# Kernel optimization log

Measured on AMD Instinct MI355X. Metric: run time of the kernel, lower is better.

The kernel has to match this reference:

```python
import jax, jax.numpy as jnp
import numpy as np

N, E = 20000, 160000
D_NODE_IN, D_EDGE_IN = 256, 64
D = 128          # node/edge feature dim
H = 256          # edge hidden dim
T = 17           # number of keypoint types
EDGE_STEPS, NODE_STEPS = 2, 1


def _w(k, shape):
    return jax.random.normal(k, shape, dtype=jnp.float32) / np.sqrt(shape[-2] if len(shape) > 1 else shape[-1]).astype(np.float32)


def setup_inputs() -> dict:
    key = jax.random.key(0)
    ks = iter(jax.random.split(key, 40))
    inp = {
        'x': jax.random.normal(next(ks), (N, D_NODE_IN), dtype=jnp.float32),
        'edge_attr': jax.random.normal(next(ks), (E, D_EDGE_IN), dtype=jnp.float32),
        'edge_index': jax.random.randint(next(ks), (2, E), 0, N),
        'node_types': jax.random.randint(next(ks), (N,), 0, T),
        # type-routed node embedding: 17 stacked 2-layer MLPs 256->128->128
        'ne_w1': _w(next(ks), (T, D_NODE_IN, D)), 'ne_b1': jnp.zeros((T, D)),
        'ne_w2': _w(next(ks), (T, D, D)),         'ne_b2': jnp.zeros((T, D)),
        # edge embedding 64->128->128
        'ee_w1': _w(next(ks), (D_EDGE_IN, D)), 'ee_b1': jnp.zeros((D,)),
        'ee_w2': _w(next(ks), (D, D)),         'ee_b2': jnp.zeros((D,)),
        # MPLayer edge MLP: [x_i, x_j, e] with skip -> (2*2D + 2D)=768 -> 256 -> 128
        'me_w1': _w(next(ks), (4 * D + 2 * D, H)), 'me_b1': jnp.zeros((H,)),
        'me_w2': _w(next(ks), (H, D)),             'me_b2': jnp.zeros((D,)),
        # MPLayer node update: [x(skip 2D), agg(D)] -> 128
        'mn_w1': _w(next(ks), (2 * D + D, D)), 'mn_b1': jnp.zeros((D,)),
        # classifiers
        'ec_w1': _w(next(ks), (D, D)), 'ec_b1': jnp.zeros((D,)),
        'ec_w2': _w(next(ks), (D, 1)), 'ec_b2': jnp.zeros((1,)),
        'nc_w1': _w(next(ks), (D, D)), 'nc_b1': jnp.zeros((D,)),
        'nc_w2': _w(next(ks), (D, 1)), 'nc_b2': jnp.zeros((1,)),
        'cc_w1': _w(next(ks), (D, D)), 'cc_b1': jnp.zeros((D,)),
        'cc_w2': _w(next(ks), (D, T)), 'cc_b2': jnp.zeros((T,)),
    }
    return inp


def _mlp2(x, w1, b1, w2, b2):
    return jax.nn.relu(x @ w1 + b1) @ w2 + b2


def reference(x, edge_attr, edge_index, node_types,
              ne_w1, ne_b1, ne_w2, ne_b2,
              ee_w1, ee_b1, ee_w2, ee_b2,
              me_w1, me_b1, me_w2, me_b2,
              mn_w1, mn_b1,
              ec_w1, ec_b1, ec_w2, ec_b2,
              nc_w1, nc_b1, nc_w2, nc_b2,
              cc_w1, cc_b1, cc_w2, cc_b2):
    n = x.shape[0]
    # NodeMlpType: run all 17 MLPs, select by node type (same math as masked dispatch)
    h = jax.nn.relu(jnp.einsum('nd,tdk->tnk', x, ne_w1) + ne_b1[:, None, :])   # [T,N,D]
    o = jnp.einsum('tnk,tkm->tnm', h, ne_w2) + ne_b2[:, None, :]               # [T,N,D]
    nf0 = o[node_types, jnp.arange(n)]                                          # [N,D]
    ef0 = _mlp2(edge_attr, ee_w1, ee_b1, ee_w2, ee_b2)                          # [E,D]

    src, dst = edge_index[0], edge_index[1]

    def mp_step(nf, ef):
        nf_c = jnp.concatenate([nf0, nf], axis=1)                               # skip concat [N,2D]
        ef_c = jnp.concatenate([ef0, ef], axis=1)                               # [E,2D]
        m = jnp.concatenate([nf_c[dst], nf_c[src], ef_c], axis=1)               # [E,6D]
        e_new = _mlp2(m, me_w1, me_b1, me_w2, me_b2)                            # [E,D]
        agg = jax.ops.segment_sum(e_new, dst, num_segments=n)                   # aggr='add'
        nf_new = jnp.concatenate([nf_c, agg], axis=1) @ mn_w1 + mn_b1           # [N,D]
        return nf_new, e_new

    nf, ef = nf0, ef0
    for _ in range(EDGE_STEPS):
        nf, ef = mp_step(nf, ef)
    pred_edge = _mlp2(ef, ec_w1, ec_b1, ec_w2, ec_b2).squeeze(-1)               # [E]
    for _ in range(NODE_STEPS):
        nf, ef = mp_step(nf, ef)
    pred_node = _mlp2(nf, nc_w1, nc_b1, nc_w2, nc_b2).squeeze(-1)               # [N]
    pred_class = _mlp2(nf, cc_w1, cc_b1, cc_w2, cc_b2)                          # [N,T]
    return (pred_edge, pred_node, pred_class, nf, ef)
```

## Files before the change

### kernel.cpp

```cpp
#include <hip/hip_runtime.h>
#include <hip/hip_bf16.h>

#define N_NODES 20000
#define N_EDGES 160000
#define DIN_NODE 256
#define DIN_EDGE 64
#define DF 128
#define HH 256
#define TT 17
#define NE_PAD_SLOTS 20544

typedef __attribute__((ext_vector_type(8))) short short8v;
typedef __attribute__((ext_vector_type(4))) float f32x4;

__device__ __forceinline__ unsigned short f2bf(float f) {
  unsigned int u = __builtin_bit_cast(unsigned int, f);
  u += 0x7FFFu + ((u >> 16) & 1u);
  return (unsigned short)(u >> 16);
}

__device__ __forceinline__ float bf2f(unsigned short u) {
  return __builtin_bit_cast(float, (unsigned int)u << 16);
}

__device__ __forceinline__ short8v pack8(float4 a, float4 b) {
  short8v o;
  o[0] = (short)f2bf(a.x); o[1] = (short)f2bf(a.y);
  o[2] = (short)f2bf(a.z); o[3] = (short)f2bf(a.w);
  o[4] = (short)f2bf(b.x); o[5] = (short)f2bf(b.y);
  o[6] = (short)f2bf(b.z); o[7] = (short)f2bf(b.w);
  return o;
}

__global__ __launch_bounds__(256) void k_pack_w(
    const float* __restrict__ w, unsigned short* __restrict__ out,
    int Kdim, int Ndim, int batch) {
  const int tile = blockIdx.x * 4 + (threadIdx.x >> 6);
  const int l = threadIdx.x & 63;
  const int ntTiles = Ndim >> 4;
  const int tilesPer = (Kdim >> 5) * ntTiles;
  if (tile >= tilesPer * batch) return;
  const int bt = tile / tilesPer;
  const int rr = tile - bt * tilesPer;
  const int kt = rr / ntTiles, nt = rr % ntTiles;
  const float* wb = w + (size_t)bt * Kdim * Ndim;
  const int col = (nt << 4) + (l & 15);
  const int k0 = (kt << 5) + ((l >> 4) << 3);
  unsigned short* o = out + (((size_t)tile << 6) + l) * 8;
#pragma unroll
  for (int j = 0; j < 8; ++j) o[j] = f2bf(wb[(size_t)(k0 + j) * Ndim + col]);
}

__global__ void k_count(const int* __restrict__ types, int* __restrict__ cnt) {
  const int n = blockIdx.x * 256 + threadIdx.x;
  if (n < N_NODES) atomicAdd(&cnt[types[n]], 1);
}
__global__ void k_prefix(const int* __restrict__ cnt, int* __restrict__ poff,
                         int* __restrict__ woff) {
  if (threadIdx.x == 0) {
    int cur = 0;
    for (int t = 0; t < TT; ++t) {
      poff[t] = cur; woff[t] = cur;
      cur += (cnt[t] + 31) & ~31;
    }
  }
}
__global__ void k_scatter(const int* __restrict__ types, int* __restrict__ woff,
                          int* __restrict__ bucket) {
  const int n = blockIdx.x * 256 + threadIdx.x;
  if (n < N_NODES) {
    const int pos = atomicAdd(&woff[types[n]], 1);
    bucket[pos] = n;
  }
}

__global__ __launch_bounds__(256) void k_node_embed_mfma(
    const float* __restrict__ x, const int* __restrict__ bucket,
    const int* __restrict__ types,
    const unsigned short* __restrict__ wp1, const float* __restrict__ b1,
    const unsigned short* __restrict__ wp2, const float* __restrict__ b2,
    unsigned short* __restrict__ nf0b) {
  __shared__ __align__(16) unsigned char A[32 * 512];
  __shared__ __align__(16) unsigned char Hb[32 * 256];
  __shared__ int sn[32];
  const int t = threadIdx.x;
  const int r0 = blockIdx.x * 32;
  if (t < 32) sn[t] = bucket[r0 + t];
  __syncthreads();
  if (sn[0] < 0) return;
  const int ty = types[sn[0]];

#pragma unroll
  for (int j = 0; j < 4; ++j) {
    const int q = j * 256 + t;
    const int i = q >> 5, c = q & 31;
    const int nd = sn[i];
    short8v o;
    if (nd >= 0) {
      const float* xr = x + (size_t)nd * DIN_NODE + c * 8;
      o = pack8(*reinterpret_cast<const float4*>(xr),
                *reinterpret_cast<const float4*>(xr + 4));
    } else {
#pragma unroll
      for (int k = 0; k < 8; ++k) o[k] = 0;
    }
    *reinterpret_cast<short8v*>(A + ((i * 512 + c * 16) ^ ((i & 7) << 4))) = o;
  }
  __syncthreads();

  const int w = t >> 6, l = t & 63, lr = l & 15, lg = l >> 4;
  const int sw = (lr & 7) << 4;
  const int row0 = lr, row1 = 16 + lr;

  f32x4 acc[2][2];
#pragma unroll
  for (int mt = 0; mt < 2; ++mt)
#pragma unroll
    for (int q = 0; q < 2; ++q)
#pragma unroll
      for (int r = 0; r < 4; ++r) acc[mt][q][r] = 0.f;

#pragma unroll
  for (int kt = 0; kt < 8; ++kt) {
    const short8v a0 = *reinterpret_cast<const short8v*>(
        A + ((row0 * 512 + kt * 64 + lg * 16) ^ sw));
    const short8v a1 = *reinterpret_cast<const short8v*>(
        A + ((row1 * 512 + kt * 64 + lg * 16) ^ sw));
#pragma unroll
    for (int q = 0; q < 2; ++q) {
      const short8v bq = *reinterpret_cast<const short8v*>(
          wp1 + (((size_t)(ty * 64 + kt * 8 + 2 * w + q) * 64 + l) << 3));
      acc[0][q] = __builtin_amdgcn_mfma_f32_16x16x32_bf16(a0, bq, acc[0][q], 0, 0, 0);
      acc[1][q] = __builtin_amdgcn_mfma_f32_16x16x32_bf16(a1, bq, acc[1][q], 0, 0, 0);
    }
  }
#pragma unroll
  for (int q = 0; q < 2; ++q) {
    const int col = (2 * w + q) * 16 + lr;
    const float bias = b1[ty * DF + col];
#pragma unroll
    for (int mt = 0; mt < 2; ++mt)
#pragma unroll
      for (int r = 0; r < 4; ++r) {
        const int row = mt * 16 + lg * 4 + r;
        *reinterpret_cast<unsigned short*>(
            Hb + ((row * 256 + col * 2) ^ ((row & 7) << 4))) =
            f2bf(fmaxf(acc[mt][q][r] + bias, 0.f));
      }
  }
  __syncthreads();

  f32x4 acc2[2][2];
#pragma unroll
  for (int mt = 0; mt < 2; ++mt)
#pragma unroll
    for (int q = 0; q < 2; ++q)
#pragma unroll
      for (int r = 0; r < 4; ++r) acc2[mt][q][r] = 0.f;
#pragma unroll
  for (int kt = 0; kt < 4; ++kt) {
    const short8v a0 = *reinterpret_cast<const short8v*>(
        Hb + ((row0 * 256 + kt * 64 + lg * 16) ^ sw));
    const short8v a1 = *reinterpret_cast<const short8v*>(
        Hb + ((row1 * 256 + kt * 64 + lg * 16) ^ sw));
#pragma unroll
    for (int q = 0; q < 2; ++q) {
      const short8v bq = *reinterpret_cast<const short8v*>(
          wp2 + (((size_t)(ty * 32 + kt * 8 + 2 * w + q) * 64 + l) << 3));
      acc2[0][q] = __builtin_amdgcn_mfma_f32_16x16x32_bf16(a0, bq, acc2[0][q], 0, 0, 0);
      acc2[1][q] = __builtin_amdgcn_mfma_f32_16x16x32_bf16(a1, bq, acc2[1][q], 0, 0, 0);
    }
  }
#pragma unroll
  for (int q = 0; q < 2; ++q) {
    const int col = (2 * w + q) * 16 + lr;
    const float bias = b2[ty * DF + col];
#pragma unroll
    for (int mt = 0; mt < 2; ++mt)
#pragma unroll
      for (int r = 0; r < 4; ++r) {
        const int row = mt * 16 + lg * 4 + r;
        const int nd = sn[row];
        if (nd >= 0)
          nf0b[(size_t)nd * DF + col] = f2bf(acc2[mt][q][r] + bias);
      }
  }
}

__global__ __launch_bounds__(256) void k_edge_embed_mfma(
    const float* __restrict__ ea,
    const unsigned short* __restrict__ wp1, const float* __restrict__ b1,
    const unsigned short* __restrict__ wp2, const float* __restrict__ b2,
    unsigned short* __restrict__ ef0b) {
  __shared__ __align__(16) unsigned char A[32 * 128];
  __shared__ __align__(16) unsigned char Hb[32 * 256];
  const int t = threadIdx.x;
  const int e0 = blockIdx.x * 32;
  {
    const int i = t >> 3, c = t & 7;
    const float* xr = ea + (size_t)(e0 + i) * DIN_EDGE + c * 8;
    const short8v o = pack8(*reinterpret_cast<const float4*>(xr),
                            *reinterpret_cast<const float4*>(xr + 4));
    *reinterpret_cast<short8v*>(A + ((i * 128 + c * 16) ^ ((i & 7) << 4))) = o;
  }
  __syncthreads();

  const int w = t >> 6, l = t & 63, lr = l & 15, lg = l >> 4;
  const int sw = (lr & 7) << 4;
  const int row0 = lr, row1 = 16 + lr;

  f32x4 acc[2][2];
#pragma unroll
  for (int mt = 0; mt < 2; ++mt)
#pragma unroll
    for (int q = 0; q < 2; ++q)
#pragma unroll
      for (int r = 0; r < 4; ++r) acc[mt][q][r] = 0.f;
#pragma unroll
  for (int kt = 0; kt < 2; ++kt) {
    const short8v a0 = *reinterpret_cast<const short8v*>(
        A + ((row0 * 128 + kt * 64 + lg * 16) ^ sw));
    const short8v a1 = *reinterpret_cast<const short8v*>(
        A + ((row1 * 128 + kt * 64 + lg * 16) ^ sw));
#pragma unroll
    for (int q = 0; q < 2; ++q) {
      const short8v bq = *reinterpret_cast<const short8v*>(
          wp1 + (((size_t)(kt * 8 + 2 * w + q) * 64 + l) << 3));
      acc[0][q] = __builtin_amdgcn_mfma_f32_16x16x32_bf16(a0, bq, acc[0][q], 0, 0, 0);
      acc[1][q] = __builtin_amdgcn_mfma_f32_16x16x32_bf16(a1, bq, acc[1][q], 0, 0, 0);
    }
  }
#pragma unroll
  for (int q = 0; q < 2; ++q) {
    const int col = (2 * w + q) * 16 + lr;
    const float bias = b1[col];
#pragma unroll
    for (int mt = 0; mt < 2; ++mt)
#pragma unroll
      for (int r = 0; r < 4; ++r) {
        const int row = mt * 16 + lg * 4 + r;
        *reinterpret_cast<unsigned short*>(
            Hb + ((row * 256 + col * 2) ^ ((row & 7) << 4))) =
            f2bf(fmaxf(acc[mt][q][r] + bias, 0.f));
      }
  }
  __syncthreads();

  f32x4 acc2[2][2];
#pragma unroll
  for (int mt = 0; mt < 2; ++mt)
#pragma unroll
    for (int q = 0; q < 2; ++q)
#pragma unroll
      for (int r = 0; r < 4; ++r) acc2[mt][q][r] = 0.f;
#pragma unroll
  for (int kt = 0; kt < 4; ++kt) {
    const short8v a0 = *reinterpret_cast<const short8v*>(
        Hb + ((row0 * 256 + kt * 64 + lg * 16) ^ sw));
    const short8v a1 = *reinterpret_cast<const short8v*>(
        Hb + ((row1 * 256 + kt * 64 + lg * 16) ^ sw));
#pragma unroll
    for (int q = 0; q < 2; ++q) {
      const short8v bq = *reinterpret_cast<const short8v*>(
          wp2 + (((size_t)(kt * 8 + 2 * w + q) * 64 + l) << 3));
      acc2[0][q] = __builtin_amdgcn_mfma_f32_16x16x32_bf16(a0, bq, acc2[0][q], 0, 0, 0);
      acc2[1][q] = __builtin_amdgcn_mfma_f32_16x16x32_bf16(a1, bq, acc2[1][q], 0, 0, 0);
    }
  }
#pragma unroll
  for (int q = 0; q < 2; ++q) {
    const int col = (2 * w + q) * 16 + lr;
    const float bias = b2[col];
#pragma unroll
    for (int mt = 0; mt < 2; ++mt)
#pragma unroll
      for (int r = 0; r < 4; ++r) {
        const int row = mt * 16 + lg * 4 + r;
        ef0b[(size_t)(e0 + row) * DF + col] = f2bf(acc2[mt][q][r] + bias);
      }
  }
}

__global__ __launch_bounds__(256) void k_partial(
    const unsigned short* __restrict__ nf0b, const unsigned short* __restrict__ nfb,
    const unsigned short* __restrict__ wpd, const unsigned short* __restrict__ wps,
    unsigned short* __restrict__ PDo, unsigned short* __restrict__ PSo) {
  __shared__ __align__(16) unsigned char A[32 * 512];
  const int t = threadIdx.x;
  const int n0 = blockIdx.x * 32;
#pragma unroll
  for (int j = 0; j < 4; ++j) {
    const int q = j * 256 + t;
    const int i = q >> 5, c = q & 31;
    const unsigned short* bp = (c < 16)
        ? nf0b + (size_t)(n0 + i) * DF + c * 8
        : nfb + (size_t)(n0 + i) * DF + (c - 16) * 8;
    *reinterpret_cast<short8v*>(A + ((i * 512 + c * 16) ^ ((i & 7) << 4))) =
        *reinterpret_cast<const short8v*>(bp);
  }
  __syncthreads();

  const int w = t >> 6, l = t & 63, lr = l & 15, lg = l >> 4;
  const int swz = (lr & 7) << 4;
  const int r0o = lr * 512 + lg * 16, r1o = (16 + lr) * 512 + lg * 16;

  f32x4 aD[2][4], aS[2][4];
#pragma unroll
  for (int mt = 0; mt < 2; ++mt)
#pragma unroll
    for (int q = 0; q < 4; ++q)
#pragma unroll
      for (int r = 0; r < 4; ++r) { aD[mt][q][r] = 0.f; aS[mt][q][r] = 0.f; }

#pragma unroll
  for (int kt = 0; kt < 8; ++kt) {
    const short8v a0 = *reinterpret_cast<const short8v*>(A + ((r0o + kt * 64) ^ swz));
    const short8v a1 = *reinterpret_cast<const short8v*>(A + ((r1o + kt * 64) ^ swz));
#pragma unroll
    for (int q = 0; q < 4; ++q) {
      const size_t bi = (((size_t)(kt * 16 + 4 * w + q) * 64 + l) << 3);
      const short8v bD = *reinterpret_cast<const short8v*>(wpd + bi);
      const short8v bS = *reinterpret_cast<const short8v*>(wps + bi);
      aD[0][q] = __builtin_amdgcn_mfma_f32_16x16x32_bf16(a0, bD, aD[0][q], 0, 0, 0);
      aD[1][q] = __builtin_amdgcn_mfma_f32_16x16x32_bf16(a1, bD, aD[1][q], 0, 0, 0);
      aS[0][q] = __builtin_amdgcn_mfma_f32_16x16x32_bf16(a0, bS, aS[0][q], 0, 0, 0);
      aS[1][q] = __builtin_amdgcn_mfma_f32_16x16x32_bf16(a1, bS, aS[1][q], 0, 0, 0);
    }
  }
#pragma unroll
  for (int q = 0; q < 4; ++q) {
    const int col = (4 * w + q) * 16 + lr;
#pragma unroll
    for (int mt = 0; mt < 2; ++mt)
#pragma unroll
      for (int r = 0; r < 4; ++r) {
        const int row = mt * 16 + lg * 4 + r;
        PDo[(size_t)(n0 + row) * HH + col] = f2bf(aD[mt][q][r]);
        PSo[(size_t)(n0 + row) * HH + col] = f2bf(aS[mt][q][r]);
      }
  }
}

template <bool OUTF>
__global__ __launch_bounds__(256) void k_edge_mlp_mfma(
    const unsigned short* __restrict__ ef0, const unsigned short* __restrict__ ef_in,
    void* __restrict__ ef_out, float* __restrict__ agg,
    const int* __restrict__ srcv, const int* __restrict__ dstv,
    const unsigned short* __restrict__ wpe, const float* __restrict__ b1,
    const unsigned short* __restrict__ wp2, const float* __restrict__ b2,
    const unsigned short* __restrict__ PDi, const unsigned short* __restrict__ PSi) {
  __shared__ __align__(16) unsigned char A_lds[32 * 512];
  __shared__ __align__(16) unsigned char P_lds[32 * 512];
  __shared__ int sd[2][32];
  const int t = threadIdx.x;
  const int e0 = blockIdx.x * 32;
  if (t < 32) sd[0][t] = srcv[e0 + t];
  else if (t < 64) sd[1][t - 32] = dstv[e0 + t - 32];

#pragma unroll
  for (int j = 0; j < 4; ++j) {
    const int q = j * 256 + t;
    const int i = q >> 5, c = q & 31;
    const unsigned short* bp = (c < 16)
        ? ef0 + (size_t)(e0 + i) * DF + c * 8
        : ef_in + (size_t)(e0 + i) * DF + (c - 16) * 8;
    *reinterpret_cast<short8v*>(A_lds + ((i * 512 + c * 16) ^ ((i & 7) << 4))) =
        *reinterpret_cast<const short8v*>(bp);
  }
  __syncthreads();

#pragma unroll
  for (int j = 0; j < 4; ++j) {
    const int q = j * 256 + t;
    const int i = q >> 5, c = q & 31;
    const short8v pd = *reinterpret_cast<const short8v*>(
        PDi + (size_t)sd[1][i] * HH + c * 8);
    const short8v ps = *reinterpret_cast<const short8v*>(
        PSi + (size_t)sd[0][i] * HH + c * 8);
    short8v o;
#pragma unroll
    for (int k = 0; k < 8; ++k)
      o[k] = (short)f2bf(bf2f((unsigned short)pd[k]) + bf2f((unsigned short)ps[k]));
    *reinterpret_cast<short8v*>(P_lds + ((i * 512 + c * 16) ^ ((i & 7) << 4))) = o;
  }
  __syncthreads();

  const int w = t >> 6, l = t & 63, lr = l & 15, lg = l >> 4;
  const int swz = (lr & 7) << 4;

  f32x4 acc[2][4];
#pragma unroll
  for (int mt = 0; mt < 2; ++mt)
#pragma unroll
    for (int q = 0; q < 4; ++q) {
      const int col = (4 * w + q) * 16 + lr;
#pragma unroll
      for (int r = 0; r < 4; ++r) {
        const int row = mt * 16 + lg * 4 + r;
        const unsigned short u = *reinterpret_cast<const unsigned short*>(
            P_lds + ((row * 512 + col * 2) ^ ((row & 7) << 4)));
        acc[mt][q][r] = bf2f(u);
      }
    }

  const int r0o = lr * 512 + lg * 16;
  const int r1o = (16 + lr) * 512 + lg * 16;
  const unsigned short* wb1 = wpe + (((size_t)(4 * w) * 64 + l) << 3);

  short8v aR[3][2], bR[3][4];
#pragma unroll
  for (int s = 0; s < 2; ++s) {
    aR[s][0] = *reinterpret_cast<const short8v*>(A_lds + ((r0o + s * 64) ^ swz));
    aR[s][1] = *reinterpret_cast<const short8v*>(A_lds + ((r1o + s * 64) ^ swz));
#pragma unroll
    for (int q = 0; q < 4; ++q)
      bR[s][q] = *reinterpret_cast<const short8v*>(wb1 + (size_t)s * 8192 + q * 512);
  }
#pragma unroll
  for (int kt = 0; kt < 8; ++kt) {
    const int cur = kt % 3, pf = (kt + 2) % 3;
    if (kt < 6) {
      aR[pf][0] = *reinterpret_cast<const short8v*>(
          A_lds + ((r0o + (kt + 2) * 64) ^ swz));
      aR[pf][1] = *reinterpret_cast<const short8v*>(
          A_lds + ((r1o + (kt + 2) * 64) ^ swz));
#pragma unroll
      for (int q = 0; q < 4; ++q)
        bR[pf][q] = *reinterpret_cast<const short8v*>(
            wb1 + (size_t)(kt + 2) * 8192 + q * 512);
    }
#pragma unroll
    for (int q = 0; q < 4; ++q) {
      acc[0][q] = __builtin_amdgcn_mfma_f32_16x16x32_bf16(aR[cur][0], bR[cur][q],
                                                          acc[0][q], 0, 0, 0);
      acc[1][q] = __builtin_amdgcn_mfma_f32_16x16x32_bf16(aR[cur][1], bR[cur][q],
                                                          acc[1][q], 0, 0, 0);
    }
  }
  __syncthreads();

#pragma unroll
  for (int q = 0; q < 4; ++q) {
    const int col = (4 * w + q) * 16 + lr;
    const float bias = b1[col];
#pragma unroll
    for (int mt = 0; mt < 2; ++mt)
#pragma unroll
      for (int r = 0; r < 4; ++r) {
        const int row = mt * 16 + lg * 4 + r;
        *reinterpret_cast<unsigned short*>(
            P_lds + ((row * 512 + col * 2) ^ ((row & 7) << 4))) =
            f2bf(fmaxf(acc[mt][q][r] + bias, 0.f));
      }
  }
  __syncthreads();

  f32x4 acc2[2][2];
#pragma unroll
  for (int mt = 0; mt < 2; ++mt)
#pragma unroll
    for (int q = 0; q < 2; ++q)
#pragma unroll
      for (int r = 0; r < 4; ++r) acc2[mt][q][r] = 0.f;

  const int h0o = lr * 512 + lg * 16;
  const int h1o = (16 + lr) * 512 + lg * 16;
  const unsigned short* wb2 = wp2 + (((size_t)(2 * w) * 64 + l) << 3);

  short8v aS[3][2], bS[3][2];
#pragma unroll
  for (int s = 0; s < 2; ++s) {
    aS[s][0] = *reinterpret_cast<const short8v*>(P_lds + ((h0o + s * 64) ^ swz));
    aS[s][1] = *reinterpret_cast<const short8v*>(P_lds + ((h1o + s * 64) ^ swz));
#pragma unroll
    for (int q = 0; q < 2; ++q)
      bS[s][q] = *reinterpret_cast<const short8v*>(wb2 + (size_t)s * 4096 + q * 512);
  }
#pragma unroll
  for (int kt = 0; kt < 8; ++kt) {
    const int cur = kt % 3, pf = (kt + 2) % 3;
    if (kt < 6) {
      aS[pf][0] = *reinterpret_cast<const short8v*>(
          P_lds + ((h0o + (kt + 2) * 64) ^ swz));
      aS[pf][1] = *reinterpret_cast<const short8v*>(
          P_lds + ((h1o + (kt + 2) * 64) ^ swz));
#pragma unroll
      for (int q = 0; q < 2; ++q)
        bS[pf][q] = *reinterpret_cast<const short8v*>(
            wb2 + (size_t)(kt + 2) * 4096 + q * 512);
    }
#pragma unroll
    for (int q = 0; q < 2; ++q) {
      acc2[0][q] = __builtin_amdgcn_mfma_f32_16x16x32_bf16(aS[cur][0], bS[cur][q],
                                                           acc2[0][q], 0, 0, 0);
      acc2[1][q] = __builtin_amdgcn_mfma_f32_16x16x32_bf16(aS[cur][1], bS[cur][q],
                                                           acc2[1][q], 0, 0, 0);
    }
  }

#pragma unroll
  for (int q = 0; q < 2; ++q) {
    const int n = (2 * w + q) * 16 + lr;
    const float bias = b2[n];
#pragma unroll
    for (int mt = 0; mt < 2; ++mt)
#pragma unroll
      for (int r = 0; r < 4; ++r) {
        const int m = mt * 16 + lg * 4 + r;
        const float v = acc2[mt][q][r] + bias;
        if (OUTF)
          ((float*)ef_out)[(size_t)(e0 + m) * DF + n] = v;
        else
          ((unsigned short*)ef_out)[(size_t)(e0 + m) * DF + n] = f2bf(v);
        atomicAdd(&agg[(size_t)sd[1][m] * DF + n], v);
      }
  }
}

template <bool OUTF>
__global__ __launch_bounds__(256) void k_node_update_mfma(
    const unsigned short* __restrict__ nf0, const unsigned short* __restrict__ nfb,
    const float* __restrict__ agg, void* __restrict__ outp,
    const unsigned short* __restrict__ wp, const float* __restrict__ b) {
  __shared__ __align__(16) unsigned char A[32 * 768];
  const int t = threadIdx.x;
  const int n0 = blockIdx.x * 32;
#pragma unroll
  for (int j = 0; j < 6; ++j) {
    const int q = j * 256 + t;
    const int i = q / 48;
    const int cc = q - i * 48;
    const int p = cc >> 4, c = cc & 15;
    const int row = n0 + i;
    short8v o;
    if (p == 0)
      o = *reinterpret_cast<const short8v*>(nf0 + (size_t)row * DF + c * 8);
    else if (p == 1)
      o = *reinterpret_cast<const short8v*>(nfb + (size_t)row * DF + c * 8);
    else {
      const float* ar = agg + (size_t)row * DF + c * 8;
      o = pack8(*reinterpret_cast<const float4*>(ar),
                *reinterpret_cast<const float4*>(ar + 4));
    }
    *reinterpret_cast<short8v*>(
        A + ((i * 768 + p * 256 + c * 16) ^ ((i & 7) << 4))) = o;
  }
  __syncthreads();

  const int w = t >> 6, l = t & 63, lr = l & 15, lg = l >> 4;
  const int sw = (lr & 7) << 4;
  const int row0 = lr, row1 = 16 + lr;

  f32x4 acc[2][2];
#pragma unroll
  for (int mt = 0; mt < 2; ++mt)
#pragma unroll
    for (int q = 0; q < 2; ++q)
#pragma unroll
      for (int r = 0; r < 4; ++r) acc[mt][q][r] = 0.f;
#pragma unroll
  for (int kt = 0; kt < 12; ++kt) {
    const short8v a0 = *reinterpret_cast<const short8v*>(
        A + ((row0 * 768 + kt * 64 + lg * 16) ^ sw));
    const short8v a1 = *reinterpret_cast<const short8v*>(
        A + ((row1 * 768 + kt * 64 + lg * 16) ^ sw));
#pragma unroll
    for (int q = 0; q < 2; ++q) {
      const short8v bq = *reinterpret_cast<const short8v*>(
          wp + (((size_t)(kt * 8 + 2 * w + q) * 64 + l) << 3));
      acc[0][q] = __builtin_amdgcn_mfma_f32_16x16x32_bf16(a0, bq, acc[0][q], 0, 0, 0);
      acc[1][q] = __builtin_amdgcn_mfma_f32_16x16x32_bf16(a1, bq, acc[1][q], 0, 0, 0);
    }
  }
#pragma unroll
  for (int q = 0; q < 2; ++q) {
    const int col = (2 * w + q) * 16 + lr;
    const float bias = b[col];
#pragma unroll
    for (int mt = 0; mt < 2; ++mt)
#pragma unroll
      for (int r = 0; r < 4; ++r) {
        const int row = mt * 16 + lg * 4 + r;
        const float v = acc[mt][q][r] + bias;
        if (OUTF)
          ((float*)outp)[(size_t)(n0 + row) * DF + col] = v;
        else
          ((unsigned short*)outp)[(size_t)(n0 + row) * DF + col] = f2bf(v);
      }
  }
}

template <bool INBF>
__global__ __launch_bounds__(256) void k_cls_scalar_mfma(
    const void* __restrict__ feat, const unsigned short* __restrict__ wp,
    const float* __restrict__ b1, const float* __restrict__ w2,
    const float* __restrict__ b2, float* __restrict__ out) {
  __shared__ __align__(16) unsigned char A[32 * 256];
  __shared__ float hid[32][136];
  __shared__ float w2s[DF];
  __shared__ float part[32][8];
  const int t = threadIdx.x;
  const int r0 = blockIdx.x * 32;
  if (t < DF) w2s[t] = w2[t];
#pragma unroll
  for (int j = 0; j < 2; ++j) {
    const int q = j * 256 + t;
    const int i = q >> 4, c = q & 15;
    short8v o;
    if (INBF) {
      o = *reinterpret_cast<const short8v*>(
          (const unsigned short*)feat + (size_t)(r0 + i) * DF + c * 8);
    } else {
      const float* fr = (const float*)feat + (size_t)(r0 + i) * DF + c * 8;
      o = pack8(*reinterpret_cast<const float4*>(fr),
                *reinterpret_cast<const float4*>(fr + 4));
    }
    *reinterpret_cast<short8v*>(A + ((i * 256 + c * 16) ^ ((i & 7) << 4))) = o;
  }
  __syncthreads();

  const int w = t >> 6, l = t & 63, lr = l & 15, lg = l >> 4;
  const int sw = (lr & 7) << 4;
  const int row0 = lr, row1 = 16 + lr;
  f32x4 acc[2][2];
#pragma unroll
  for (int mt = 0; mt < 2; ++mt)
#pragma unroll
    for (int q = 0; q < 2; ++q)
#pragma unroll
      for (int r = 0; r < 4; ++r) acc[mt][q][r] = 0.f;
#pragma unroll
  for (int kt = 0; kt < 4; ++kt) {
    const short8v a0 = *reinterpret_cast<const short8v*>(
        A + ((row0 * 256 + kt * 64 + lg * 16) ^ sw));
    const short8v a1 = *reinterpret_cast<const short8v*>(
        A + ((row1 * 256 + kt * 64 + lg * 16) ^ sw));
#pragma unroll
    for (int q = 0; q < 2; ++q) {
      const short8v bq = *reinterpret_cast<const short8v*>(
          wp + (((size_t)(kt * 8 + 2 * w + q) * 64 + l) << 3));
      acc[0][q] = __builtin_amdgcn_mfma_f32_16x16x32_bf16(a0, bq, acc[0][q], 0, 0, 0);
      acc[1][q] = __builtin_amdgcn_mfma_f32_16x16x32_bf16(a1, bq, acc[1][q], 0, 0, 0);
    }
  }
#pragma unroll
  for (int q = 0; q < 2; ++q) {
    const int col = (2 * w + q) * 16 + lr;
    const float bias = b1[col];
#pragma unroll
    for (int mt = 0; mt < 2; ++mt)
#pragma unroll
      for (int r = 0; r < 4; ++r) {
        const int row = mt * 16 + lg * 4 + r;
        hid[row][col] = fmaxf(acc[mt][q][r] + bias, 0.f);
      }
  }
  __syncthreads();
  {
    const int r = t >> 3, kc = t & 7;
    float s = 0.f;
#pragma unroll
    for (int u = 0; u < 16; ++u) s = fmaf(hid[r][kc * 16 + u], w2s[kc * 16 + u], s);
    part[r][kc] = s;
  }
  __syncthreads();
  if (t < 32) {
    float s = b2[0];
#pragma unroll
    for (int k = 0; k < 8; ++k) s += part[t][k];
    out[r0 + t] = s;
  }
}

__global__ __launch_bounds__(256) void k_cls_class_mfma(
    const float* __restrict__ feat, const unsigned short* __restrict__ wp,
    const float* __restrict__ b1, const float* __restrict__ w2,
    const float* __restrict__ b2, float* __restrict__ out) {
  __shared__ __align__(16) unsigned char A[32 * 256];
  __shared__ float hid[32][136];
  __shared__ float w2s[DF * TT];
  const int t = threadIdx.x;
  const int r0 = blockIdx.x * 32;
  for (int j = t; j < DF * TT; j += 256) w2s[j] = w2[j];
#pragma unroll
  for (int j = 0; j < 2; ++j) {
    const int q = j * 256 + t;
    const int i = q >> 4, c = q & 15;
    const float* fr = feat + (size_t)(r0 + i) * DF + c * 8;
    const short8v o = pack8(*reinterpret_cast<const float4*>(fr),
                            *reinterpret_cast<const float4*>(fr + 4));
    *reinterpret_cast<short8v*>(A + ((i * 256 + c * 16) ^ ((i & 7) << 4))) = o;
  }
  __syncthreads();

  const int w = t >> 6, l = t & 63, lr = l & 15, lg = l >> 4;
  const int sw = (lr & 7) << 4;
  const int row0 = lr, row1 = 16 + lr;
  f32x4 acc[2][2];
#pragma unroll
  for (int mt = 0; mt < 2; ++mt)
#pragma unroll
    for (int q = 0; q < 2; ++q)
#pragma unroll
      for (int r = 0; r < 4; ++r) acc[mt][q][r] = 0.f;
#pragma unroll
  for (int kt = 0; kt < 4; ++kt) {
    const short8v a0 = *reinterpret_cast<const short8v*>(
        A + ((row0 * 256 + kt * 64 + lg * 16) ^ sw));
    const short8v a1 = *reinterpret_cast<const short8v*>(
        A + ((row1 * 256 + kt * 64 + lg * 16) ^ sw));
#pragma unroll
    for (int q = 0; q < 2; ++q) {
      const short8v bq = *reinterpret_cast<const short8v*>(
          wp + (((size_t)(kt * 8 + 2 * w + q) * 64 + l) << 3));
      acc[0][q] = __builtin_amdgcn_mfma_f32_16x16x32_bf16(a0, bq, acc[0][q], 0, 0, 0);
      acc[1][q] = __builtin_amdgcn_mfma_f32_16x16x32_bf16(a1, bq, acc[1][q], 0, 0, 0);
    }
  }
#pragma unroll
  for (int q = 0; q < 2; ++q) {
    const int col = (2 * w + q) * 16 + lr;
    const float bias = b1[col];
#pragma unroll
    for (int mt = 0; mt < 2; ++mt)
#pragma unroll
      for (int r = 0; r < 4; ++r) {
        const int row = mt * 16 + lg * 4 + r;
        hid[row][col] = fmaxf(acc[mt][q][r] + bias, 0.f);
      }
  }
  __syncthreads();
  for (int o = t; o < 32 * TT; o += 256) {
    const int r = o / TT, c = o - TT * r;
    float s = b2[c];
    for (int k = 0; k < DF; ++k) s = fmaf(hid[r][k], w2s[k * TT + c], s);
    out[(size_t)(r0 + r) * TT + c] = s;
  }
}

extern "C" void kernel_launch(void* const* d_in, const int* in_sizes, int n_in,
                              void* d_out, int out_size, void* d_ws,
                              size_t ws_size, hipStream_t stream) {
  (void)in_sizes; (void)n_in; (void)out_size; (void)ws_size;
  const float* x         = (const float*)d_in[0];
  const float* edge_attr = (const float*)d_in[1];
  const int*   edge_idx  = (const int*)d_in[2];
  const int*   node_ty   = (const int*)d_in[3];
  const float* ne_w1 = (const float*)d_in[4];
  const float* ne_b1 = (const float*)d_in[5];
  const float* ne_w2 = (const float*)d_in[6];
  const float* ne_b2 = (const float*)d_in[7];
  const float* ee_w1 = (const float*)d_in[8];
  const float* ee_b1 = (const float*)d_in[9];
  const float* ee_w2 = (const float*)d_in[10];
  const float* ee_b2 = (const float*)d_in[11];
  const float* me_w1 = (const float*)d_in[12];
  const float* me_b1 = (const float*)d_in[13];
  const float* me_w2 = (const float*)d_in[14];
  const float* me_b2 = (const float*)d_in[15];
  const float* mn_w1 = (const float*)d_in[16];
  const float* mn_b1 = (const float*)d_in[17];
  const float* ec_w1 = (const float*)d_in[18];
  const float* ec_b1 = (const float*)d_in[19];
  const float* ec_w2 = (const float*)d_in[20];
  const float* ec_b2 = (const float*)d_in[21];
  const float* nc_w1 = (const float*)d_in[22];
  const float* nc_b1 = (const float*)d_in[23];
  const float* nc_w2 = (const float*)d_in[24];
  const float* nc_b2 = (const float*)d_in[25];
  const float* cc_w1 = (const float*)d_in[26];
  const float* cc_b1 = (const float*)d_in[27];
  const float* cc_w2 = (const float*)d_in[28];
  const float* cc_b2 = (const float*)d_in[29];

  const int* srcv = edge_idx;
  const int* dstv = edge_idx + N_EDGES;

  float* agg = (float*)d_ws;
  unsigned short* nf0b = (unsigned short*)(agg + (size_t)N_NODES * DF);
  unsigned short* nf1b = nf0b + (size_t)N_NODES * DF;
  unsigned short* ef0b = nf1b + (size_t)N_NODES * DF;
  unsigned short* ef1b = ef0b + (size_t)N_EDGES * DF;
  unsigned short* wmpD = ef1b + (size_t)N_EDGES * DF;
  unsigned short* wmpS = wmpD + 256 * 256;
  unsigned short* wmeE = wmpS + 256 * 256;
  unsigned short* wme2 = wmeE + 256 * 256;
  unsigned short* wmn  = wme2 + 256 * 128;
  unsigned short* wne1 = wmn + 384 * 128;
  unsigned short* wne2 = wne1 + (size_t)TT * 256 * 128;
  unsigned short* wee1 = wne2 + (size_t)TT * 128 * 128;
  unsigned short* wee2 = wee1 + 64 * 128;
  unsigned short* wec  = wee2 + 128 * 128;
  unsigned short* wnc  = wec + 128 * 128;
  unsigned short* wcc  = wnc + 128 * 128;
  unsigned short* PD   = wcc + 128 * 128;
  unsigned short* PS   = PD + (size_t)N_NODES * HH;
  int* cnt    = (int*)(PS + (size_t)N_NODES * HH);
  int* poff   = cnt + 32;
  int* woff   = poff + 32;
  int* bucket = woff + 32;

  float* out_pe = (float*)d_out;
  float* out_pn = out_pe + N_EDGES;
  float* out_pc = out_pn + N_NODES;
  float* out_nf = out_pc + (size_t)N_NODES * TT;
  float* out_ef = out_nf + (size_t)N_NODES * DF;

  k_pack_w<<<32, 256, 0, stream>>>(me_w1, wmpD, 256, 256, 1);
  k_pack_w<<<32, 256, 0, stream>>>(me_w1 + 256 * 256, wmpS, 256, 256, 1);
  k_pack_w<<<32, 256, 0, stream>>>(me_w1 + 512 * 256, wmeE, 256, 256, 1);
  k_pack_w<<<16, 256, 0, stream>>>(me_w2, wme2, 256, 128, 1);
  k_pack_w<<<24, 256, 0, stream>>>(mn_w1, wmn, 384, 128, 1);
  k_pack_w<<<272, 256, 0, stream>>>(ne_w1, wne1, 256, 128, TT);
  k_pack_w<<<136, 256, 0, stream>>>(ne_w2, wne2, 128, 128, TT);
  k_pack_w<<<4, 256, 0, stream>>>(ee_w1, wee1, 64, 128, 1);
  k_pack_w<<<8, 256, 0, stream>>>(ee_w2, wee2, 128, 128, 1);
  k_pack_w<<<8, 256, 0, stream>>>(ec_w1, wec, 128, 128, 1);
  k_pack_w<<<8, 256, 0, stream>>>(nc_w1, wnc, 128, 128, 1);
  k_pack_w<<<8, 256, 0, stream>>>(cc_w1, wcc, 128, 128, 1);

  hipMemsetAsync(cnt, 0, 32 * sizeof(int), stream);
  hipMemsetAsync(bucket, 0xFF, NE_PAD_SLOTS * sizeof(int), stream);
  k_count<<<(N_NODES + 255) / 256, 256, 0, stream>>>(node_ty, cnt);
  k_prefix<<<1, 64, 0, stream>>>(cnt, poff, woff);
  k_scatter<<<(N_NODES + 255) / 256, 256, 0, stream>>>(node_ty, woff, bucket);

  k_node_embed_mfma<<<NE_PAD_SLOTS / 32, 256, 0, stream>>>(
      x, bucket, node_ty, wne1, ne_b1, wne2, ne_b2, nf0b);
  k_edge_embed_mfma<<<N_EDGES / 32, 256, 0, stream>>>(edge_attr, wee1, ee_b1,
                                                      wee2, ee_b2, ef0b);

  hipMemsetAsync(agg, 0, (size_t)N_NODES * DF * sizeof(float), stream);
  k_partial<<<N_NODES / 32, 256, 0, stream>>>(nf0b, nf0b, wmpD, wmpS, PD, PS);
  k_edge_mlp_mfma<false><<<N_EDGES / 32, 256, 0, stream>>>(
      ef0b, ef0b, (void*)ef1b, agg, srcv, dstv, wmeE, me_b1, wme2, me_b2, PD, PS);
  k_node_update_mfma<false><<<N_NODES / 32, 256, 0, stream>>>(
      nf0b, nf0b, agg, (void*)nf1b, wmn, mn_b1);
  hipMemsetAsync(agg, 0, (size_t)N_NODES * DF * sizeof(float), stream);
  k_partial<<<N_NODES / 32, 256, 0, stream>>>(nf0b, nf1b, wmpD, wmpS, PD, PS);
  k_edge_mlp_mfma<false><<<N_EDGES / 32, 256, 0, stream>>>(
      ef0b, ef1b, (void*)ef1b, agg, srcv, dstv, wmeE, me_b1, wme2, me_b2, PD, PS);
  k_node_update_mfma<false><<<N_NODES / 32, 256, 0, stream>>>(
      nf0b, nf1b, agg, (void*)nf1b, wmn, mn_b1);
  k_cls_scalar_mfma<true><<<N_EDGES / 32, 256, 0, stream>>>(
      (const void*)ef1b, wec, ec_b1, ec_w2, ec_b2, out_pe);
  hipMemsetAsync(agg, 0, (size_t)N_NODES * DF * sizeof(float), stream);
  k_partial<<<N_NODES / 32, 256, 0, stream>>>(nf0b, nf1b, wmpD, wmpS, PD, PS);
  k_edge_mlp_mfma<true><<<N_EDGES / 32, 256, 0, stream>>>(
      ef0b, ef1b, (void*)out_ef, agg, srcv, dstv, wmeE, me_b1, wme2, me_b2, PD, PS);
  k_node_update_mfma<true><<<N_NODES / 32, 256, 0, stream>>>(
      nf0b, nf1b, agg, (void*)out_nf, wmn, mn_b1);

  k_cls_scalar_mfma<false><<<N_NODES / 32, 256, 0, stream>>>(
      (const void*)out_nf, wnc, nc_b1, nc_w2, nc_b2, out_pn);
  k_cls_class_mfma<<<N_NODES / 32, 256, 0, stream>>>(out_nf, wcc, cc_b1, cc_w2,
                                                     cc_b2, out_pc);
}
```

Baseline: 633.1 us.

## Replace atomic scatter aggregation with CSR gather and fuse partials and edge head

Builds a destination-sorted CSR edge list once, using degree count, scan and scatter kernels. Each node update then gathers and sums its incoming edge rows instead of the edge MLP doing float atomicAdds into a zeroed agg buffer. The node-update kernel also computes the next step's PD/PS partial projections, and the second edge MLP computes the edge classifier head in place. This removes the separate partial, classifier and memset launches and the atomic traffic. In exchange it adds irregular per-node gather loops with degree-dependent load imbalance, a serial single-block scan, and more register and LDS pressure in the fused kernels.

```diff
diff --git a/kernel.cpp b/kernel.cpp
--- a/kernel.cpp
+++ b/kernel.cpp
@@ -74,6 +74,48 @@
   }
 }
 
+__global__ void k_deg(const int* __restrict__ dstv, int* __restrict__ deg) {
+  const int e = blockIdx.x * 256 + threadIdx.x;
+  if (e < N_EDGES) atomicAdd(&deg[dstv[e]], 1);
+}
+__global__ __launch_bounds__(256) void k_scan(const int* __restrict__ deg,
+                                              int* __restrict__ rs,
+                                              int* __restrict__ wo) {
+  __shared__ int partial[256];
+  const int t = threadIdx.x;
+  const int base = t * 80;
+  int s = 0;
+  for (int j = 0; j < 80; ++j) {
+    const int n = base + j;
+    if (n < N_NODES) s += deg[n];
+  }
+  partial[t] = s;
+  __syncthreads();
+  for (int off = 1; off < 256; off <<= 1) {
+    const int v = (t >= off) ? partial[t - off] : 0;
+    __syncthreads();
+    partial[t] += v;
+    __syncthreads();
+  }
+  int run = (t > 0) ? partial[t - 1] : 0;
+  for (int j = 0; j < 80; ++j) {
+    const int n = base + j;
+    if (n < N_NODES) {
+      rs[n] = run; wo[n] = run;
+      run += deg[n];
+    }
+  }
+  if (t == 255) rs[N_NODES] = run;
+}
+__global__ void k_elist(const int* __restrict__ dstv, int* __restrict__ wo,
+                        int* __restrict__ elist) {
+  const int e = blockIdx.x * 256 + threadIdx.x;
+  if (e < N_EDGES) {
+    const int pos = atomicAdd(&wo[dstv[e]], 1);
+    elist[pos] = e;
+  }
+}
+
 __global__ __launch_bounds__(256) void k_node_embed_mfma(
     const float* __restrict__ x, const int* __restrict__ bucket,
     const int* __restrict__ types,
@@ -341,17 +383,21 @@
   }
 }
 
-template <bool OUTF>
+template <bool OUTF, bool HEAD>
 __global__ __launch_bounds__(256) void k_edge_mlp_mfma(
     const unsigned short* __restrict__ ef0, const unsigned short* __restrict__ ef_in,
-    void* __restrict__ ef_out, float* __restrict__ agg,
+    void* __restrict__ ef_out,
     const int* __restrict__ srcv, const int* __restrict__ dstv,
     const unsigned short* __restrict__ wpe, const float* __restrict__ b1,
     const unsigned short* __restrict__ wp2, const float* __restrict__ b2,
-    const unsigned short* __restrict__ PDi, const unsigned short* __restrict__ PSi) {
+    const unsigned short* __restrict__ PDi, const unsigned short* __restrict__ PSi,
+    const unsigned short* __restrict__ wech, const float* __restrict__ hb1,
+    const float* __restrict__ hw2, const float* __restrict__ hb2,
+    float* __restrict__ out_pe) {
   __shared__ __align__(16) unsigned char A_lds[32 * 512];
   __shared__ __align__(16) unsigned char P_lds[32 * 512];
   __shared__ int sd[2][32];
+  __shared__ float hpart[32][8];
   const int t = threadIdx.x;
   const int e0 = blockIdx.x * 32;
   if (t < 32) sd[0][t] = srcv[e0 + t];
@@ -512,38 +558,141 @@
           ((float*)ef_out)[(size_t)(e0 + m) * DF + n] = v;
         else
           ((unsigned short*)ef_out)[(size_t)(e0 + m) * DF + n] = f2bf(v);
-        atomicAdd(&agg[(size_t)sd[1][m] * DF + n], v);
-      }
-  }
-}
-
-template <bool OUTF>
+      }
+  }
+
+  if constexpr (HEAD) {
+    __syncthreads();
+#pragma unroll
+    for (int q = 0; q < 2; ++q) {
+      const int n = (2 * w + q) * 16 + lr;
+      const float bias = b2[n];
+#pragma unroll
+      for (int mt = 0; mt < 2; ++mt)
+#pragma unroll
+        for (int r = 0; r < 4; ++r) {
+          const int m = mt * 16 + lg * 4 + r;
+          *reinterpret_cast<unsigned short*>(
+              P_lds + ((m * 256 + n * 2) ^ ((m & 7) << 4))) =
+              f2bf(acc2[mt][q][r] + bias);
+        }
+    }
+    __syncthreads();
+    f32x4 ah[2][2];
+#pragma unroll
+    for (int mt = 0; mt < 2; ++mt)
+#pragma unroll
+      for (int q = 0; q < 2; ++q)
+#pragma unroll
+        for (int r = 0; r < 4; ++r) ah[mt][q][r] = 0.f;
+#pragma unroll
+    for (int kt = 0; kt < 4; ++kt) {
+      const short8v a0 = *reinterpret_cast<const short8v*>(
+          P_lds + ((lr * 256 + kt * 64 + lg * 16) ^ swz));
+      const short8v a1 = *reinterpret_cast<const short8v*>(
+          P_lds + (((16 + lr) * 256 + kt * 64 + lg * 16) ^ swz));
+#pragma unroll
+      for (int q = 0; q < 2; ++q) {
+        const short8v bq = *reinterpret_cast<const short8v*>(
+            wech + (((size_t)(kt * 8 + 2 * w + q) * 64 + l) << 3));
+        ah[0][q] = __builtin_amdgcn_mfma_f32_16x16x32_bf16(a0, bq, ah[0][q], 0, 0, 0);
+        ah[1][q] = __builtin_amdgcn_mfma_f32_16x16x32_bf16(a1, bq, ah[1][q], 0, 0, 0);
+      }
+    }
+#pragma unroll
+    for (int q = 0; q < 2; ++q) {
+      const int col = (2 * w + q) * 16 + lr;
+      const float bias = hb1[col];
+#pragma unroll
+      for (int mt = 0; mt < 2; ++mt)
+#pragma unroll
+        for (int r = 0; r < 4; ++r) {
+          const int row = mt * 16 + lg * 4 + r;
+          *reinterpret_cast<unsigned short*>(A_lds + row * 256 + col * 2) =
+              f2bf(fmaxf(ah[mt][q][r] + bias, 0.f));
+        }
+    }
+    __syncthreads();
+    {
+      const int rr = t >> 3, kc = t & 7;
+      float s = 0.f;
+#pragma unroll
+      for (int u = 0; u < 16; ++u)
+        s = fmaf(bf2f(*reinterpret_cast<const unsigned short*>(
+                     A_lds + rr * 256 + (kc * 16 + u) * 2)),
+                 hw2[kc * 16 + u], s);
+      hpart[rr][kc] = s;
+    }
+    __syncthreads();
+    if (t < 32) {
+      float s = hb2[0];
+#pragma unroll
+      for (int k = 0; k < 8; ++k) s += hpart[t][k];
+      out_pe[e0 + t] = s;
+    }
+  }
+}
+
+template <bool OUTF, bool PART>
 __global__ __launch_bounds__(256) void k_node_update_mfma(
     const unsigned short* __restrict__ nf0, const unsigned short* __restrict__ nfb,
-    const float* __restrict__ agg, void* __restrict__ outp,
-    const unsigned short* __restrict__ wp, const float* __restrict__ b) {
+    const void* __restrict__ efrows,
+    const int* __restrict__ rs, const int* __restrict__ elist,
+    void* __restrict__ outp,
+    const unsigned short* __restrict__ wp, const float* __restrict__ b,
+    const unsigned short* __restrict__ wpd, const unsigned short* __restrict__ wps,
+    unsigned short* __restrict__ PDo, unsigned short* __restrict__ PSo) {
   __shared__ __align__(16) unsigned char A[32 * 768];
   const int t = threadIdx.x;
   const int n0 = blockIdx.x * 32;
 #pragma unroll
-  for (int j = 0; j < 6; ++j) {
+  for (int j = 0; j < 4; ++j) {
     const int q = j * 256 + t;
-    const int i = q / 48;
-    const int cc = q - i * 48;
-    const int p = cc >> 4, c = cc & 15;
-    const int row = n0 + i;
-    short8v o;
-    if (p == 0)
-      o = *reinterpret_cast<const short8v*>(nf0 + (size_t)row * DF + c * 8);
-    else if (p == 1)
-      o = *reinterpret_cast<const short8v*>(nfb + (size_t)row * DF + c * 8);
-    else {
-      const float* ar = agg + (size_t)row * DF + c * 8;
-      o = pack8(*reinterpret_cast<const float4*>(ar),
-                *reinterpret_cast<const float4*>(ar + 4));
-    }
-    *reinterpret_cast<short8v*>(
-        A + ((i * 768 + p * 256 + c * 16) ^ ((i & 7) << 4))) = o;
+    const int i = q >> 5, c = q & 31;
+    const unsigned short* bp = (c < 16)
+        ? nf0 + (size_t)(n0 + i) * DF + c * 8
+        : nfb + (size_t)(n0 + i) * DF + (c - 16) * 8;
+    *reinterpret_cast<short8v*>(A + ((i * 768 + c * 16) ^ ((i & 7) << 4))) =
+        *reinterpret_cast<const short8v*>(bp);
+  }
+  {
+    const int i = t >> 3, sub = t & 7;
+    const int n = n0 + i;
+    const int kb = rs[n], ke = rs[n + 1];
+    float av[16];
+#pragma unroll
+    for (int u = 0; u < 16; ++u) av[u] = 0.f;
+    for (int k = kb; k < ke; ++k) {
+      const int e = elist[k];
+      if (OUTF) {
+        const float* er = (const float*)efrows + (size_t)e * DF + sub * 16;
+#pragma unroll
+        for (int u4 = 0; u4 < 4; ++u4) {
+          const float4 f = *reinterpret_cast<const float4*>(er + u4 * 4);
+          av[u4 * 4 + 0] += f.x; av[u4 * 4 + 1] += f.y;
+          av[u4 * 4 + 2] += f.z; av[u4 * 4 + 3] += f.w;
+        }
+      } else {
+        const unsigned short* er =
+            (const unsigned short*)efrows + (size_t)e * DF + sub * 16;
+        const short8v v0 = *reinterpret_cast<const short8v*>(er);
+        const short8v v1 = *reinterpret_cast<const short8v*>(er + 8);
+#pragma unroll
+        for (int u = 0; u < 8; ++u) {
+          av[u] += bf2f((unsigned short)v0[u]);
+          av[8 + u] += bf2f((unsigned short)v1[u]);
+        }
+      }
+    }
+    short8v o0, o1;
+#pragma unroll
+    for (int u = 0; u < 8; ++u) {
+      o0[u] = (short)f2bf(av[u]);
+      o1[u] = (short)f2bf(av[8 + u]);
+    }
+    const int c0 = 32 + sub * 2;
+    *reinterpret_cast<short8v*>(A + ((i * 768 + c0 * 16) ^ ((i & 7) << 4))) = o0;
+    *reinterpret_cast<short8v*>(A + ((i * 768 + (c0 + 1) * 16) ^ ((i & 7) << 4))) = o1;
   }
   __syncthreads();
 
@@ -587,6 +736,60 @@
         else
           ((unsigned short*)outp)[(size_t)(n0 + row) * DF + col] = f2bf(v);
       }
+  }
+
+  if constexpr (PART) {
+    __syncthreads();
+#pragma unroll
+    for (int q = 0; q < 2; ++q) {
+      const int col = (2 * w + q) * 16 + lr;
+      const float bias = b[col];
+#pragma unroll
+      for (int mt = 0; mt < 2; ++mt)
+#pragma unroll
+        for (int r = 0; r < 4; ++r) {
+          const int row = mt * 16 + lg * 4 + r;
+          *reinterpret_cast<unsigned short*>(
+              A + ((row * 768 + 256 + col * 2) ^ ((row & 7) << 4))) =
+              f2bf(acc[mt][q][r] + bias);
+        }
+    }
+    __syncthreads();
+    f32x4 aD[2][4], aSv[2][4];
+#pragma unroll
+    for (int mt = 0; mt < 2; ++mt)
+#pragma unroll
+      for (int q = 0; q < 4; ++q)
+#pragma unroll
+        for (int r = 0; r < 4; ++r) { aD[mt][q][r] = 0.f; aSv[mt][q][r] = 0.f; }
+    const int r0p = lr * 768 + lg * 16, r1p = (16 + lr) * 768 + lg * 16;
+#pragma unroll
+    for (int kt = 0; kt < 8; ++kt) {
+      const short8v a0 = *reinterpret_cast<const short8v*>(A + ((r0p + kt * 64) ^ sw));
+      const short8v a1 = *reinterpret_cast<const short8v*>(A + ((r1p + kt * 64) ^ sw));
+#pragma unroll
+      for (int q = 0; q < 4; ++q) {
+        const size_t bi = (((size_t)(kt * 16 + 4 * w + q) * 64 + l) << 3);
+        const short8v bD = *reinterpret_cast<const short8v*>(wpd + bi);
+        const short8v bSv = *reinterpret_cast<const short8v*>(wps + bi);
+        aD[0][q] = __builtin_amdgcn_mfma_f32_16x16x32_bf16(a0, bD, aD[0][q], 0, 0, 0);
+        aD[1][q] = __builtin_amdgcn_mfma_f32_16x16x32_bf16(a1, bD, aD[1][q], 0, 0, 0);
+        aSv[0][q] = __builtin_amdgcn_mfma_f32_16x16x32_bf16(a0, bSv, aSv[0][q], 0, 0, 0);
+        aSv[1][q] = __builtin_amdgcn_mfma_f32_16x16x32_bf16(a1, bSv, aSv[1][q], 0, 0, 0);
+      }
+    }
+#pragma unroll
+    for (int q = 0; q < 4; ++q) {
+      const int col = (4 * w + q) * 16 + lr;
+#pragma unroll
+      for (int mt = 0; mt < 2; ++mt)
+#pragma unroll
+        for (int r = 0; r < 4; ++r) {
+          const int row = mt * 16 + lg * 4 + r;
+          PDo[(size_t)(n0 + row) * HH + col] = f2bf(aD[mt][q][r]);
+          PSo[(size_t)(n0 + row) * HH + col] = f2bf(aSv[mt][q][r]);
+        }
+    }
   }
 }
 
@@ -776,8 +979,7 @@
   const int* srcv = edge_idx;
   const int* dstv = edge_idx + N_EDGES;
 
-  float* agg = (float*)d_ws;
-  unsigned short* nf0b = (unsigned short*)(agg + (size_t)N_NODES * DF);
+  unsigned short* nf0b = (unsigned short*)d_ws;
   unsigned short* nf1b = nf0b + (size_t)N_NODES * DF;
   unsigned short* ef0b = nf1b + (size_t)N_NODES * DF;
   unsigned short* ef1b = ef0b + (size_t)N_EDGES * DF;
@@ -799,6 +1001,10 @@
   int* poff   = cnt + 32;
   int* woff   = poff + 32;
   int* bucket = woff + 32;
+  int* deg    = bucket + NE_PAD_SLOTS;
+  int* rs     = deg + N_NODES;
+  int* wo     = rs + N_NODES + 1;
+  int* elist  = wo + N_NODES;
 
   float* out_pe = (float*)d_out;
   float* out_pn = out_pe + N_EDGES;
@@ -825,31 +1031,35 @@
   k_prefix<<<1, 64, 0, stream>>>(cnt, poff, woff);
   k_scatter<<<(N_NODES + 255) / 256, 256, 0, stream>>>(node_ty, woff, bucket);
 
+  hipMemsetAsync(deg, 0, N_NODES * sizeof(int), stream);
+  k_deg<<<(N_EDGES + 255) / 256, 256, 0, stream>>>(dstv, deg);
+  k_scan<<<1, 256, 0, stream>>>(deg, rs, wo);
+  k_elist<<<(N_EDGES + 255) / 256, 256, 0, stream>>>(dstv, wo, elist);
+
   k_node_embed_mfma<<<NE_PAD_SLOTS / 32, 256, 0, stream>>>(
       x, bucket, node_ty, wne1, ne_b1, wne2, ne_b2, nf0b);
   k_edge_embed_mfma<<<N_EDGES / 32, 256, 0, stream>>>(edge_attr, wee1, ee_b1,
                                                       wee2, ee_b2, ef0b);
 
-  hipMemsetAsync(agg, 0, (size_t)N_NODES * DF * sizeof(float), stream);
   k_partial<<<N_NODES / 32, 256, 0, stream>>>(nf0b, nf0b, wmpD, wmpS, PD, PS);
-  k_edge_mlp_mfma<false><<<N_EDGES / 32, 256, 0, stream>>>(
-      ef0b, ef0b, (void*)ef1b, agg, srcv, dstv, wmeE, me_b1, wme2, me_b2, PD, PS);
-  k_node_update_mfma<false><<<N_NODES / 32, 256, 0, stream>>>(
-      nf0b, nf0b, agg, (void*)nf1b, wmn, mn_b1);
-  hipMemsetAsync(agg, 0, (size_t)N_NODES * DF * sizeof(float), stream);
-  k_partial<<<N_NODES / 32, 256, 0, stream>>>(nf0b, nf1b, wmpD, wmpS, PD, PS);
-  k_edge_mlp_mfma<false><<<N_EDGES / 32, 256, 0, stream>>>(
-      ef0b, ef1b, (void*)ef1b, agg, srcv, dstv, wmeE, me_b1, wme2, me_b2, PD, PS);
-  k_node_update_mfma<false><<<N_NODES / 32, 256, 0, stream>>>(
-      nf0b, nf1b, agg, (void*)nf1b, wmn, mn_b1);
-  k_cls_scalar_mfma<true><<<N_EDGES / 32, 256, 0, stream>>>(
-      (const void*)ef1b, wec, ec_b1, ec_w2, ec_b2, out_pe);
-  hipMemsetAsync(agg, 0, (size_t)N_NODES * DF * sizeof(float), stream);
-  k_partial<<<N_NODES / 32, 256, 0, stream>>>(nf0b, nf1b, wmpD, wmpS, PD, PS);
-  k_edge_mlp_mfma<true><<<N_EDGES / 32, 256, 0, stream>>>(
-      ef0b, ef1b, (void*)out_ef, agg, srcv, dstv, wmeE, me_b1, wme2, me_b2, PD, PS);
-  k_node_update_mfma<true><<<N_NODES / 32, 256, 0, stream>>>(
-      nf0b, nf1b, agg, (void*)out_nf, wmn, mn_b1);
+  k_edge_mlp_mfma<false, false><<<N_EDGES / 32, 256, 0, stream>>>(
+      ef0b, ef0b, (void*)ef1b, srcv, dstv, wmeE, me_b1, wme2, me_b2, PD, PS,
+      nullptr, nullptr, nullptr, nullptr, nullptr);
+  k_node_update_mfma<false, true><<<N_NODES / 32, 256, 0, stream>>>(
+      nf0b, nf0b, (const void*)ef1b, rs, elist, (void*)nf1b, wmn, mn_b1,
+      wmpD, wmpS, PD, PS);
+  k_edge_mlp_mfma<false, true><<<N_EDGES / 32, 256, 0, stream>>>(
+      ef0b, ef1b, (void*)ef1b, srcv, dstv, wmeE, me_b1, wme2, me_b2, PD, PS,
+      wec, ec_b1, ec_w2, ec_b2, out_pe);
+  k_node_update_mfma<false, true><<<N_NODES / 32, 256, 0, stream>>>(
+      nf0b, nf1b, (const void*)ef1b, rs, elist, (void*)nf1b, wmn, mn_b1,
+      wmpD, wmpS, PD, PS);
+  k_edge_mlp_mfma<true, false><<<N_EDGES / 32, 256, 0, stream>>>(
+      ef0b, ef1b, (void*)out_ef, srcv, dstv, wmeE, me_b1, wme2, me_b2, PD, PS,
+      nullptr, nullptr, nullptr, nullptr, nullptr);
+  k_node_update_mfma<true, false><<<N_NODES / 32, 256, 0, stream>>>(
+      nf0b, nf1b, (const void*)out_ef, rs, elist, (void*)out_nf, wmn, mn_b1,
+      wmpD, wmpS, PD, PS);
 
   k_cls_scalar_mfma<false><<<N_NODES / 32, 256, 0, stream>>>(
       (const void*)out_nf, wnc, nc_b1, nc_w2, nc_b2, out_pn);
```

After: 651.3 us. +2.9%, slower.
